# Kernel tuning notes

Measured on AMD Instinct MI355X. Metric: run time of the kernel, lower is better.

Reference implementation:

```python
import jax, jax.numpy as jnp
import numpy as np

# alpha clamp limits: balance=False -> [exp(-1/5), exp(-1/25)]
ALPHA_MIN = float(np.exp(-1.0 / 5.0))
ALPHA_MAX = float(np.exp(-1.0 / 25.0))
T_CROP = 100


def setup_inputs() -> dict:
    key = jax.random.key(0)
    k1, k2, k3 = jax.random.split(key, 3)
    B, T, D, H = 128, 1000, 1024, 256
    x = jax.random.normal(k1, (B, T, D), dtype=jnp.float32)
    bound = float(np.sqrt(1.0 / D))
    W = jax.random.uniform(k2, (H, D), minval=-bound, maxval=bound, dtype=jnp.float32)
    alpha = jax.random.uniform(k3, (H,), minval=ALPHA_MIN, maxval=ALPHA_MAX, dtype=jnp.float32)
    return {"x": x, "W": W, "alpha": alpha}


def reference(x, W, alpha):
    # x: [B, T, D], W: [H, D], alpha: [H]
    a = jnp.clip(alpha, ALPHA_MIN, ALPHA_MAX)
    Wx = jnp.einsum('btd,hd->bth', x, W)  # [B, T, H]
    T = Wx.shape[1]
    mask = (jnp.arange(T) >= T_CROP).astype(Wx.dtype)  # [T]
    Wx_t = jnp.moveaxis(Wx, 1, 0)  # [T, B, H]

    def step(carry, inp):
        ut, out = carry
        wx, m = inp
        ut = a * ut + (1.0 - a) * wx
        out = out + m * jax.nn.softmax(ut, axis=-1)
        return (ut, out), None

    B, H = Wx.shape[0], Wx.shape[2]
    init = (jnp.zeros((B, H), Wx.dtype), jnp.zeros((B, H), Wx.dtype))
    (_, out), _ = jax.lax.scan(step, init, (Wx_t, mask))
    return out  # [B, H]
```

## Files before the change

kernel.cpp:

```cpp
#include <hip/hip_runtime.h>
#include <hip/hip_bf16.h>

#define B_    128
#define T_    1000
#define D_    1024
#define H_    256
#define TCROP 100
#define CHUNK 50
#define NCH   20
#define CSKIP 2

typedef __attribute__((ext_vector_type(8))) short bfrag8;
typedef __attribute__((ext_vector_type(4))) float f32x4;
typedef unsigned long long ull;

__device__ __forceinline__ unsigned short f2bf(float f) {
    union { float f; unsigned int u; } v; v.f = f;
    unsigned int u = v.u;
    u += 0x7FFFu + ((u >> 16) & 1u);
    return (unsigned short)(u >> 16);
}
__device__ __forceinline__ float bf2f(unsigned short u) {
    union { unsigned int u; float f; } v; v.u = ((unsigned int)u) << 16;
    return v.f;
}
__device__ __forceinline__ unsigned int pack2(float lo, float hi) {
    union { float f; unsigned int u; } a, b; a.f = lo; b.f = hi;
    return __builtin_amdgcn_perm(b.u + 0x8000u, a.u + 0x8000u, 0x07060302u);
}
__device__ __forceinline__ bfrag8 cvt8(float4 f0, float4 f1) {
    union { bfrag8 v; unsigned int u[4]; } r;
    r.u[0] = pack2(f0.x, f0.y);
    r.u[1] = pack2(f0.z, f0.w);
    r.u[2] = pack2(f1.x, f1.y);
    r.u[3] = pack2(f1.z, f1.w);
    return r.v;
}

__global__ __launch_bounds__(256) void wconv_kernel(
        const float* __restrict__ W, unsigned short* __restrict__ Wbf) {
    const int i = (blockIdx.x * 256 + threadIdx.x) * 8;
    float4 f0 = *(const float4*)(W + i);
    float4 f1 = *(const float4*)(W + i + 4);
    *(bfrag8*)(Wbf + i) = cvt8(f0, f1);
}

__global__ __launch_bounds__(512) void gemm_kernel(
        const float* __restrict__ x, const unsigned short* __restrict__ Wbf,
        unsigned short* __restrict__ Wx) {
    __shared__ unsigned short smem[32768];
    unsigned short* As = smem;
    unsigned short* Bs = smem + 128 * 64;

    const int tid  = threadIdx.x;
    const int lane = tid & 63;
    const int wave = tid >> 6;
    const int wr   = wave >> 2;
    const int wc   = wave & 3;
    const int m0   = blockIdx.x * 128;

    f32x4 acc[4][4];
#pragma unroll
    for (int m = 0; m < 4; ++m)
#pragma unroll
        for (int n = 0; n < 4; ++n) acc[m][n] = (f32x4){0.f, 0.f, 0.f, 0.f};

    const int rr  = lane & 15;
    const int kh  = lane >> 4;
    const int ra0 = tid >> 3;
    const int ja  = tid & 7;
    const int sa  = (ja ^ (ra0 & 7)) * 8;

    for (int kt = 0; kt < D_; kt += 64) {
#pragma unroll
        for (int q = 0; q < 4; ++q) {
            const int li = q * 512 + tid;
            const int r  = li >> 3;
            const int j  = li & 7;
            const int jj = j ^ (r & 7);
            const unsigned short* src = Wbf + (size_t)r * D_ + kt + jj * 8;
            unsigned short* dst = &Bs[li * 8];
            __builtin_amdgcn_global_load_lds(
                (const __attribute__((address_space(1))) void*)src,
                (__attribute__((address_space(3))) void*)dst, 16, 0, 0);
        }
#pragma unroll
        for (int q = 0; q < 2; ++q) {
            const int r = ra0 + q * 64;
            const float* src = x + (size_t)(m0 + r) * D_ + kt + ja * 8;
            float4 f0 = *(const float4*)src;
            float4 f1 = *(const float4*)(src + 4);
            *(bfrag8*)&As[r * 64 + sa] = cvt8(f0, f1);
        }
        __syncthreads();

#pragma unroll
        for (int kk = 0; kk < 2; ++kk) {
            const int c16 = kk * 4 + kh;
            bfrag8 af[4], bfr[4];
#pragma unroll
            for (int m = 0; m < 4; ++m) {
                const int row = wr * 64 + m * 16 + rr;
                af[m] = *(const bfrag8*)&As[row * 64 + ((c16 ^ (row & 7)) * 8)];
            }
#pragma unroll
            for (int n = 0; n < 4; ++n) {
                const int row = wc * 64 + n * 16 + rr;
                bfr[n] = *(const bfrag8*)&Bs[row * 64 + ((c16 ^ (row & 7)) * 8)];
            }
#pragma unroll
            for (int m = 0; m < 4; ++m)
#pragma unroll
                for (int n = 0; n < 4; ++n)
                    acc[m][n] = __builtin_amdgcn_mfma_f32_16x16x32_bf16(
                        af[m], bfr[n], acc[m][n], 0, 0, 0);
        }
        __syncthreads();
    }

    const int cl = lane & 15, rg = lane >> 4;
#pragma unroll
    for (int m = 0; m < 4; ++m)
#pragma unroll
        for (int n = 0; n < 4; ++n)
#pragma unroll
            for (int j = 0; j < 4; ++j) {
                const int row = wr * 64 + m * 16 + rg * 4 + j;
                const int col = wc * 64 + n * 16 + cl;
                smem[row * 256 + (col ^ (((row >> 2) & 3) << 4))] =
                    f2bf(acc[m][n][j]);
            }
    __syncthreads();
#pragma unroll
    for (int li = tid; li < 4096; li += 512) {
        const int r  = li >> 5;
        const int cg = (li & 31) * 8;
        const int scg = cg ^ (((r >> 2) & 3) << 4);
        bfrag8 v = *(const bfrag8*)&smem[r * 256 + scg];
        *(bfrag8*)&Wx[(size_t)(m0 + r) * H_ + cg] = v;
    }
}

__global__ __launch_bounds__(64) void scanA_kernel(
        const unsigned short* __restrict__ Wx, const float* __restrict__ alpha,
        float* __restrict__ F) {
    const int c = blockIdx.x, b = blockIdx.y;
    const int lane = threadIdx.x;
    const int h = lane * 4;

    const float AMIN = 0.81873075307798182f, AMAX = 0.96078943915232320f;
    float4 al = *(const float4*)(alpha + h);
    float a[4]  = {fminf(fmaxf(al.x, AMIN), AMAX), fminf(fmaxf(al.y, AMIN), AMAX),
                   fminf(fmaxf(al.z, AMIN), AMAX), fminf(fmaxf(al.w, AMIN), AMAX)};
    float om[4] = {1.f - a[0], 1.f - a[1], 1.f - a[2], 1.f - a[3]};

    float ut[4] = {0.f, 0.f, 0.f, 0.f};
    const unsigned short* base = Wx + ((size_t)b * T_ + c * CHUNK) * H_ + h;
#pragma unroll 10
    for (int t = 0; t < CHUNK; ++t) {
        ull wv = *(const ull*)(base + (size_t)t * H_);
        ut[0] = a[0] * ut[0] + om[0] * bf2f((unsigned short)wv);
        ut[1] = a[1] * ut[1] + om[1] * bf2f((unsigned short)(wv >> 16));
        ut[2] = a[2] * ut[2] + om[2] * bf2f((unsigned short)(wv >> 32));
        ut[3] = a[3] * ut[3] + om[3] * bf2f((unsigned short)(wv >> 48));
    }
    float4 o; o.x = ut[0]; o.y = ut[1]; o.z = ut[2]; o.w = ut[3];
    *(float4*)(F + ((size_t)b * NCH + c) * H_ + h) = o;
}

__global__ __launch_bounds__(256) void scanB_kernel(
        const float* __restrict__ F, const float* __restrict__ alpha,
        float* __restrict__ S) {
    const int b = blockIdx.x, h = threadIdx.x;
    const float AMIN = 0.81873075307798182f, AMAX = 0.96078943915232320f;
    const float a = fminf(fmaxf(alpha[h], AMIN), AMAX);
    const float aL = powf(a, (float)CHUNK);
    float f[NCH];
#pragma unroll
    for (int c = 0; c < NCH; ++c)
        f[c] = F[((size_t)b * NCH + c) * H_ + h];
    float s = 0.f;
#pragma unroll
    for (int c = 0; c < NCH; ++c) {
        S[((size_t)b * NCH + c) * H_ + h] = s;
        s = aL * s + f[c];
    }
}

__global__ __launch_bounds__(64) void scanC_kernel(
        const unsigned short* __restrict__ Wx, const float* __restrict__ alpha,
        const float* __restrict__ S, float* __restrict__ P) {
    const int c = blockIdx.x + CSKIP;
    const int b = blockIdx.y;
    const int lane = threadIdx.x;
    const int h = lane * 4;

    const float AMIN = 0.81873075307798182f, AMAX = 0.96078943915232320f;
    float4 al = *(const float4*)(alpha + h);
    float a[4]  = {fminf(fmaxf(al.x, AMIN), AMAX), fminf(fmaxf(al.y, AMIN), AMAX),
                   fminf(fmaxf(al.z, AMIN), AMAX), fminf(fmaxf(al.w, AMIN), AMAX)};
    float om[4] = {1.f - a[0], 1.f - a[1], 1.f - a[2], 1.f - a[3]};

    float4 s0 = *(const float4*)(S + ((size_t)b * NCH + c) * H_ + h);
    float ut[4]   = {s0.x, s0.y, s0.z, s0.w};
    float acc4[4] = {0.f, 0.f, 0.f, 0.f};

    const unsigned short* base = Wx + ((size_t)b * T_ + c * CHUNK) * H_ + h;
#pragma unroll
    for (int tb = 0; tb < CHUNK; tb += 5) {
        float e[5][4], sl[5];
#pragma unroll
        for (int q = 0; q < 5; ++q) {
            ull wv = *(const ull*)(base + (size_t)(tb + q) * H_);
            ut[0] = a[0] * ut[0] + om[0] * bf2f((unsigned short)wv);
            ut[1] = a[1] * ut[1] + om[1] * bf2f((unsigned short)(wv >> 16));
            ut[2] = a[2] * ut[2] + om[2] * bf2f((unsigned short)(wv >> 32));
            ut[3] = a[3] * ut[3] + om[3] * bf2f((unsigned short)(wv >> 48));
            e[q][0] = __expf(ut[0]);
            e[q][1] = __expf(ut[1]);
            e[q][2] = __expf(ut[2]);
            e[q][3] = __expf(ut[3]);
            sl[q] = (e[q][0] + e[q][1]) + (e[q][2] + e[q][3]);
        }
#pragma unroll
        for (int dd = 1; dd < 64; dd <<= 1) {
            sl[0] += __shfl_xor(sl[0], dd);
            sl[1] += __shfl_xor(sl[1], dd);
            sl[2] += __shfl_xor(sl[2], dd);
            sl[3] += __shfl_xor(sl[3], dd);
            sl[4] += __shfl_xor(sl[4], dd);
        }
#pragma unroll
        for (int q = 0; q < 5; ++q) {
            const float rcp = 1.0f / sl[q];
            acc4[0] += e[q][0] * rcp;
            acc4[1] += e[q][1] * rcp;
            acc4[2] += e[q][2] * rcp;
            acc4[3] += e[q][3] * rcp;
        }
    }
    float4 o; o.x = acc4[0]; o.y = acc4[1]; o.z = acc4[2]; o.w = acc4[3];
    *(float4*)(P + ((size_t)b * NCH + c) * H_ + h) = o;
}

__global__ __launch_bounds__(256) void scanD_kernel(
        const float* __restrict__ P, float* __restrict__ out) {
    const int b = blockIdx.x, h = threadIdx.x;
    float s = 0.f;
    for (int c = CSKIP; c < NCH; ++c) s += P[((size_t)b * NCH + c) * H_ + h];
    out[(size_t)b * H_ + h] = s;
}

extern "C" void kernel_launch(void* const* d_in, const int* in_sizes, int n_in,
                              void* d_out, int out_size, void* d_ws, size_t ws_size,
                              hipStream_t stream) {
    const float* x     = (const float*)d_in[0];
    const float* W     = (const float*)d_in[1];
    const float* alpha = (const float*)d_in[2];
    float* out = (float*)d_out;

    char* ws = (char*)d_ws;
    unsigned short* Wbf = (unsigned short*)ws;
    unsigned short* Wx  = (unsigned short*)(ws + ((size_t)1 << 20));
    float* F = (float*)(ws + ((size_t)70 << 20));
    float* S = (float*)(ws + ((size_t)80 << 20));
    float* P = (float*)(ws + ((size_t)90 << 20));

    wconv_kernel<<<128, 256, 0, stream>>>(W, Wbf);
    gemm_kernel<<<(B_ * T_) / 128, 512, 0, stream>>>(x, Wbf, Wx);
    scanA_kernel<<<dim3(NCH, B_), 64, 0, stream>>>(Wx, alpha, F);
    scanB_kernel<<<B_, H_, 0, stream>>>(F, alpha, S);
    scanC_kernel<<<dim3(NCH - CSKIP, B_), 64, 0, stream>>>(Wx, alpha, S, P);
    scanD_kernel<<<B_, 256, 0, stream>>>(P, out);
}
```

Measured before the change: 174.1 us.

## Double-buffer GEMM shared-memory tiles to overlap global loads with MFMA

Converts the GEMM K-loop to a double-buffered software pipeline. The next K-tile of W goes straight to LDS through async global_load_lds, and the next x tile is prefetched into registers while the MFMAs run on the current buffer. Each iteration now needs one barrier instead of two. In exchange, shared memory grows to 96KB per block and register pressure rises from the prefetched x values, which may affect occupancy.

```diff
diff --git a/kernel.cpp b/kernel.cpp
--- a/kernel.cpp
+++ b/kernel.cpp
@@ -48,9 +48,7 @@
 __global__ __launch_bounds__(512) void gemm_kernel(
         const float* __restrict__ x, const unsigned short* __restrict__ Wbf,
         unsigned short* __restrict__ Wx) {
-    __shared__ unsigned short smem[32768];
-    unsigned short* As = smem;
-    unsigned short* Bs = smem + 128 * 64;
+    __shared__ unsigned short smem[49152];
 
     const int tid  = threadIdx.x;
     const int lane = tid & 63;
@@ -70,30 +68,55 @@
     const int ra0 = tid >> 3;
     const int ja  = tid & 7;
     const int sa  = (ja ^ (ra0 & 7)) * 8;
-
-    for (int kt = 0; kt < D_; kt += 64) {
+    const float* ap0 = x + (size_t)(m0 + ra0) * D_ + ja * 8;
+    const float* ap1 = ap0 + (size_t)64 * D_;
+
+    {
+        float4 f00 = *(const float4*)ap0;
+        float4 f01 = *(const float4*)(ap0 + 4);
+        float4 f10 = *(const float4*)ap1;
+        float4 f11 = *(const float4*)(ap1 + 4);
 #pragma unroll
         for (int q = 0; q < 4; ++q) {
             const int li = q * 512 + tid;
             const int r  = li >> 3;
             const int j  = li & 7;
             const int jj = j ^ (r & 7);
-            const unsigned short* src = Wbf + (size_t)r * D_ + kt + jj * 8;
-            unsigned short* dst = &Bs[li * 8];
             __builtin_amdgcn_global_load_lds(
-                (const __attribute__((address_space(1))) void*)src,
-                (__attribute__((address_space(3))) void*)dst, 16, 0, 0);
-        }
-#pragma unroll
-        for (int q = 0; q < 2; ++q) {
-            const int r = ra0 + q * 64;
-            const float* src = x + (size_t)(m0 + r) * D_ + kt + ja * 8;
-            float4 f0 = *(const float4*)src;
-            float4 f1 = *(const float4*)(src + 4);
-            *(bfrag8*)&As[r * 64 + sa] = cvt8(f0, f1);
-        }
-        __syncthreads();
-
+                (const __attribute__((address_space(1))) void*)
+                    (Wbf + (size_t)r * D_ + jj * 8),
+                (__attribute__((address_space(3))) void*)&smem[16384 + li * 8],
+                16, 0, 0);
+        }
+        *(bfrag8*)&smem[ra0 * 64 + sa]        = cvt8(f00, f01);
+        *(bfrag8*)&smem[(ra0 + 64) * 64 + sa] = cvt8(f10, f11);
+    }
+    __syncthreads();
+
+    for (int it = 0; it < 16; ++it) {
+        const int cur = it & 1, nxt = cur ^ 1;
+        float4 f00, f01, f10, f11;
+        if (it < 15) {
+            const int ktn = (it + 1) * 64;
+#pragma unroll
+            for (int q = 0; q < 4; ++q) {
+                const int li = q * 512 + tid;
+                const int r  = li >> 3;
+                const int j  = li & 7;
+                const int jj = j ^ (r & 7);
+                __builtin_amdgcn_global_load_lds(
+                    (const __attribute__((address_space(1))) void*)
+                        (Wbf + (size_t)r * D_ + ktn + jj * 8),
+                    (__attribute__((address_space(3))) void*)
+                        &smem[16384 + nxt * 16384 + li * 8], 16, 0, 0);
+            }
+            f00 = *(const float4*)(ap0 + ktn);
+            f01 = *(const float4*)(ap0 + ktn + 4);
+            f10 = *(const float4*)(ap1 + ktn);
+            f11 = *(const float4*)(ap1 + ktn + 4);
+        }
+        const unsigned short* Asb = smem + cur * 8192;
+        const unsigned short* Bsb = smem + 16384 + cur * 16384;
 #pragma unroll
         for (int kk = 0; kk < 2; ++kk) {
             const int c16 = kk * 4 + kh;
@@ -101,12 +124,12 @@
 #pragma unroll
             for (int m = 0; m < 4; ++m) {
                 const int row = wr * 64 + m * 16 + rr;
-                af[m] = *(const bfrag8*)&As[row * 64 + ((c16 ^ (row & 7)) * 8)];
+                af[m] = *(const bfrag8*)&Asb[row * 64 + ((c16 ^ (row & 7)) * 8)];
             }
 #pragma unroll
             for (int n = 0; n < 4; ++n) {
                 const int row = wc * 64 + n * 16 + rr;
-                bfr[n] = *(const bfrag8*)&Bs[row * 64 + ((c16 ^ (row & 7)) * 8)];
+                bfr[n] = *(const bfrag8*)&Bsb[row * 64 + ((c16 ^ (row & 7)) * 8)];
             }
 #pragma unroll
             for (int m = 0; m < 4; ++m)
@@ -114,6 +137,11 @@
                 for (int n = 0; n < 4; ++n)
                     acc[m][n] = __builtin_amdgcn_mfma_f32_16x16x32_bf16(
                         af[m], bfr[n], acc[m][n], 0, 0, 0);
+        }
+        if (it < 15) {
+            unsigned short* Asn = smem + nxt * 8192;
+            *(bfrag8*)&Asn[ra0 * 64 + sa]        = cvt8(f00, f01);
+            *(bfrag8*)&Asn[(ra0 + 64) * 64 + sa] = cvt8(f10, f11);
         }
         __syncthreads();
     }
```

Result: slower. 188.3 us (+8.2%).

## Fuse chunk-local scan pass into GEMM epilogue using shared-memory tile

Applied to the files above, without the earlier changes.

Removes the scanA kernel by having half the GEMM block's threads run the per-chunk linear recurrence directly over the bf16 tile in shared memory, while the other half write Wx out. Because 128-row GEMM tiles do not align with 50-step chunks, each chunk may be split across two tiles, so partial segment sums are stored and scanB recombines them with a power-of-alpha correction. This avoids re-reading Wx from global memory and one kernel launch. In exchange it adds a serial 128-step loop to the GEMM epilogue and halves the threads doing the store.

```diff
diff --git a/kernel.cpp b/kernel.cpp
--- a/kernel.cpp
+++ b/kernel.cpp
@@ -47,7 +47,8 @@
 
 __global__ __launch_bounds__(512) void gemm_kernel(
         const float* __restrict__ x, const unsigned short* __restrict__ Wbf,
-        unsigned short* __restrict__ Wx) {
+        const float* __restrict__ alpha,
+        unsigned short* __restrict__ Wx, float* __restrict__ Seg) {
     __shared__ unsigned short smem[32768];
     unsigned short* As = smem;
     unsigned short* Bs = smem + 128 * 64;
@@ -131,59 +132,56 @@
                     f2bf(acc[m][n][j]);
             }
     __syncthreads();
-#pragma unroll
-    for (int li = tid; li < 4096; li += 512) {
-        const int r  = li >> 5;
-        const int cg = (li & 31) * 8;
-        const int scg = cg ^ (((r >> 2) & 3) << 4);
-        bfrag8 v = *(const bfrag8*)&smem[r * 256 + scg];
-        *(bfrag8*)&Wx[(size_t)(m0 + r) * H_ + cg] = v;
-    }
-}
-
-__global__ __launch_bounds__(64) void scanA_kernel(
-        const unsigned short* __restrict__ Wx, const float* __restrict__ alpha,
-        float* __restrict__ F) {
-    const int c = blockIdx.x, b = blockIdx.y;
-    const int lane = threadIdx.x;
-    const int h = lane * 4;
-
-    const float AMIN = 0.81873075307798182f, AMAX = 0.96078943915232320f;
-    float4 al = *(const float4*)(alpha + h);
-    float a[4]  = {fminf(fmaxf(al.x, AMIN), AMAX), fminf(fmaxf(al.y, AMIN), AMAX),
-                   fminf(fmaxf(al.z, AMIN), AMAX), fminf(fmaxf(al.w, AMIN), AMAX)};
-    float om[4] = {1.f - a[0], 1.f - a[1], 1.f - a[2], 1.f - a[3]};
-
-    float ut[4] = {0.f, 0.f, 0.f, 0.f};
-    const unsigned short* base = Wx + ((size_t)b * T_ + c * CHUNK) * H_ + h;
-#pragma unroll 10
-    for (int t = 0; t < CHUNK; ++t) {
-        ull wv = *(const ull*)(base + (size_t)t * H_);
-        ut[0] = a[0] * ut[0] + om[0] * bf2f((unsigned short)wv);
-        ut[1] = a[1] * ut[1] + om[1] * bf2f((unsigned short)(wv >> 16));
-        ut[2] = a[2] * ut[2] + om[2] * bf2f((unsigned short)(wv >> 32));
-        ut[3] = a[3] * ut[3] + om[3] * bf2f((unsigned short)(wv >> 48));
-    }
-    float4 o; o.x = ut[0]; o.y = ut[1]; o.z = ut[2]; o.w = ut[3];
-    *(float4*)(F + ((size_t)b * NCH + c) * H_ + h) = o;
+
+    if (tid < 256) {
+        const int h = tid;
+        const float AMIN = 0.81873075307798182f, AMAX = 0.96078943915232320f;
+        const float a  = fminf(fmaxf(alpha[h], AMIN), AMAX);
+        const float om = 1.0f - a;
+        float ut = 0.f;
+        int g = m0 / CHUNK;
+        int segstart = 0;
+        for (int r = 0; r < 128; ++r) {
+            ut = a * ut + om * bf2f(smem[r * 256 + (h ^ (((r >> 2) & 3) << 4))]);
+            if (((m0 + r) % CHUNK) == (CHUNK - 1) || r == 127) {
+                const int which = ((m0 + segstart) % CHUNK == 0) ? 0 : 1;
+                Seg[((size_t)g * 2 + which) * H_ + h] = ut;
+                ut = 0.f;
+                ++g;
+                segstart = r + 1;
+            }
+        }
+    } else {
+        for (int li = tid - 256; li < 4096; li += 256) {
+            const int r  = li >> 5;
+            const int cg = (li & 31) * 8;
+            const int scg = cg ^ (((r >> 2) & 3) << 4);
+            bfrag8 v = *(const bfrag8*)&smem[r * 256 + scg];
+            *(bfrag8*)&Wx[(size_t)(m0 + r) * H_ + cg] = v;
+        }
+    }
 }
 
 __global__ __launch_bounds__(256) void scanB_kernel(
-        const float* __restrict__ F, const float* __restrict__ alpha,
+        const float* __restrict__ Seg, const float* __restrict__ alpha,
         float* __restrict__ S) {
     const int b = blockIdx.x, h = threadIdx.x;
     const float AMIN = 0.81873075307798182f, AMAX = 0.96078943915232320f;
     const float a = fminf(fmaxf(alpha[h], AMIN), AMAX);
-    const float aL = powf(a, (float)CHUNK);
-    float f[NCH];
-#pragma unroll
-    for (int c = 0; c < NCH; ++c)
-        f[c] = F[((size_t)b * NCH + c) * H_ + h];
+    const float aL = __powf(a, (float)CHUNK);
     float s = 0.f;
 #pragma unroll
     for (int c = 0; c < NCH; ++c) {
         S[((size_t)b * NCH + c) * H_ + h] = s;
-        s = aL * s + f[c];
+        const int g  = b * NCH + c;
+        const int cs = g * CHUNK;
+        const int p  = ((cs >> 7) + 1) << 7;
+        float F = Seg[((size_t)g * 2) * H_ + h];
+        if (p < cs + CHUNK) {
+            const int len1 = cs + CHUNK - p;
+            F = __powf(a, (float)len1) * F + Seg[((size_t)g * 2 + 1) * H_ + h];
+        }
+        s = aL * s + F;
     }
 }
 
@@ -262,14 +260,13 @@
     char* ws = (char*)d_ws;
     unsigned short* Wbf = (unsigned short*)ws;
     unsigned short* Wx  = (unsigned short*)(ws + ((size_t)1 << 20));
-    float* F = (float*)(ws + ((size_t)70 << 20));
-    float* S = (float*)(ws + ((size_t)80 << 20));
-    float* P = (float*)(ws + ((size_t)90 << 20));
+    float* Seg = (float*)(ws + ((size_t)70 << 20));
+    float* S   = (float*)(ws + ((size_t)80 << 20));
+    float* P   = (float*)(ws + ((size_t)90 << 20));
 
     wconv_kernel<<<128, 256, 0, stream>>>(W, Wbf);
-    gemm_kernel<<<(B_ * T_) / 128, 512, 0, stream>>>(x, Wbf, Wx);
-    scanA_kernel<<<dim3(NCH, B_), 64, 0, stream>>>(Wx, alpha, F);
-    scanB_kernel<<<B_, H_, 0, stream>>>(F, alpha, S);
+    gemm_kernel<<<(B_ * T_) / 128, 512, 0, stream>>>(x, Wbf, alpha, Wx, Seg);
+    scanB_kernel<<<B_, H_, 0, stream>>>(Seg, alpha, S);
     scanC_kernel<<<dim3(NCH - CSKIP, B_), 64, 0, stream>>>(Wx, alpha, S, P);
     scanD_kernel<<<B_, 256, 0, stream>>>(P, out);
 }
```

After: 184.4 us. +5.9%, slower.
